# Optimization experiments

Hardware: AMD Instinct MI355X
Metric: run time of the kernel (lower is better)

Reference implementation:

```python
import jax, jax.numpy as jnp
import numpy as np

K = 1024
D = 64
BETA = 0.25


def setup_inputs() -> dict:
    key = jax.random.key(0)
    k1, k2 = jax.random.split(key)
    latents = jax.random.normal(k1, (32, 64, 64, 64), dtype=jnp.float32)  # [B, C=D, H, W]
    # embedding init: uniform(-1/K, 1/K)
    embedding = jax.random.uniform(k2, (K, D), dtype=jnp.float32, minval=-1.0 / K, maxval=1.0 / K)
    return {"latents": latents, "embedding": embedding}


def reference(latents, embedding):
    # [B, D, H, W] -> [B, H, W, D]
    x = jnp.transpose(latents, (0, 2, 3, 1))
    shp = x.shape
    flat = x.reshape(-1, D)  # [N, D]

    dist = (jnp.sum(flat ** 2, axis=1, keepdims=True)
            + jnp.sum(embedding ** 2, axis=1)
            - 2.0 * flat @ embedding.T)  # [N, K]
    inds = jnp.argmin(dist, axis=1)  # [N]

    quantized = embedding[inds].reshape(shp)  # gather == one-hot @ embedding

    commitment_loss = jnp.mean((jax.lax.stop_gradient(quantized) - x) ** 2)
    embedding_loss = jnp.mean((quantized - jax.lax.stop_gradient(x)) ** 2)
    vq_loss = commitment_loss * BETA + embedding_loss

    # straight-through estimator
    quantized = x + jax.lax.stop_gradient(quantized - x)
    out = jnp.transpose(quantized, (0, 3, 1, 2))  # back to [B, D, H, W]
    return out, vq_loss
```

## Files before the change

### kernel.cpp

```cpp
#include <hip/hip_runtime.h>
#include <hip/hip_bf16.h>


#define HW 4096
#define OUTELEMS 8388608

typedef __attribute__((ext_vector_type(8))) short bf16x8;
typedef __attribute__((ext_vector_type(4))) float f32x4;
typedef __attribute__((ext_vector_type(4))) int i32x4;

static __device__ __forceinline__ short f2bf(float f) {
    union { __hip_bfloat16 h; short s; } u;
    u.h = __float2bfloat16(f);
    return u.s;
}
static __device__ __forceinline__ unsigned umin2(unsigned a, unsigned b) {
    return a < b ? a : b;
}


__global__ __launch_bounds__(256) void prep_kernel(const float* __restrict__ emb,
                                                   short* __restrict__ Ebf,
                                                   float* __restrict__ en1,
                                                   float* __restrict__ loss) {
    int code = blockIdx.x * 4 + (threadIdx.x >> 6);
    int d = threadIdx.x & 63;
    float v = emb[code * 64 + d];
    int g = d >> 3, j = d & 7;
    Ebf[code * 64 + ((g + code) & 7) * 8 + j] = f2bf(-2.0f * v);
    float s = v * v;
#pragma unroll
    for (int off = 32; off > 0; off >>= 1) s += __shfl_xor(s, off, 64);
    if (d == 0) en1[code] = 1.0f + s;
    if (blockIdx.x == 0 && threadIdx.x == 0) *loss = 0.0f;
}

__global__ __launch_bounds__(512, 2) void vq_kernel(
        const float* __restrict__ lat, const short* __restrict__ Ebf,
        const float* __restrict__ en1, float* __restrict__ out,
        float* __restrict__ loss) {
    extern __shared__ __align__(16) char sbuf[];
    const int tid  = threadIdx.x;
    const int wave = tid >> 6;
    const int lane = tid & 63;
    const int n    = lane & 15;
    const int quad = lane >> 4;

    const int g0 = blockIdx.x * 512;
    const int b  = g0 >> 12;
    const int mb = g0 & 4095;
    const float* latb = lat + (size_t)b * 262144;

    {
        const f32x4* src = (const f32x4*)Ebf;
        f32x4* dst = (f32x4*)sbuf;
#pragma unroll
        for (int r = 0; r < 16; ++r)
            dst[r * 512 + tid] = src[r * 512 + tid];
        if (tid < 256)
            ((f32x4*)(sbuf + 131072))[tid] = ((const f32x4*)en1)[tid];
    }

    bf16x8 bfr[4][2];
    float xnorm[4];
#pragma unroll
    for (int s = 0; s < 4; ++s) {
        const float* xp = latb + (mb + wave * 64 + s * 16 + n);
        float xs = 0.0f; bf16x8 f0, f1;
#pragma unroll
        for (int j = 0; j < 8; ++j) {
            float x0 = xp[(quad * 8 + j) * HW];
            float x1 = xp[(32 + quad * 8 + j) * HW];
            xs += x0 * x0 + x1 * x1;
            f0[j] = f2bf(x0); f1[j] = f2bf(x1);
        }
        bfr[s][0] = f0; bfr[s][1] = f1; xnorm[s] = xs;
    }
    __syncthreads();

    const int slot0 = ((quad + n) & 7) * 16;
    const int slot1 = ((quad + 4 + n) & 7) * 16;
    const char* arowBase = sbuf + n * 128;
    const f32x4* enl = (const f32x4*)(sbuf + 131072);
    unsigned emin[4] = {0xFFFFFFFFu, 0xFFFFFFFFu, 0xFFFFFFFFu, 0xFFFFFFFFu};

#pragma unroll 2
    for (int ct = 0; ct < 64; ++ct) {
        const char* rb = arowBase + ct * 2048;
        bf16x8 a0 = *(const bf16x8*)(rb + slot0);
        bf16x8 a1 = *(const bf16x8*)(rb + slot1);
        f32x4 en4 = enl[ct * 4 + quad];
        const unsigned cb = ct * 16 + quad * 4;
#pragma unroll
        for (int s = 0; s < 4; ++s) {
            f32x4 acc = __builtin_amdgcn_mfma_f32_16x16x32_bf16(a0, bfr[s][0], en4, 0, 0, 0);
            acc = __builtin_amdgcn_mfma_f32_16x16x32_bf16(a1, bfr[s][1], acc, 0, 0, 0);
            unsigned e0 = (__float_as_uint(acc[0]) & 0xFFFFFC00u) | (cb + 0);
            unsigned e1 = (__float_as_uint(acc[1]) & 0xFFFFFC00u) | (cb + 1);
            unsigned e2 = (__float_as_uint(acc[2]) & 0xFFFFFC00u) | (cb + 2);
            unsigned e3 = (__float_as_uint(acc[3]) & 0xFFFFFC00u) | (cb + 3);
            emin[s] = umin2(emin[s], umin2(umin2(e0, e1), umin2(e2, e3)));
        }
    }

#pragma unroll
    for (int off = 16; off <= 32; off <<= 1) {
#pragma unroll
        for (int s = 0; s < 4; ++s) {
            unsigned eo = (unsigned)__shfl_xor((int)emin[s], off, 64);
            float xo = __shfl_xor(xnorm[s], off, 64);
            emin[s] = eo < emin[s] ? eo : emin[s];
            xnorm[s] += xo;
        }
    }

    int* codes = (int*)(sbuf + 135168);
    if (quad == 0) {
#pragma unroll
        for (int s = 0; s < 4; ++s)
            codes[wave * 64 + s * 16 + n] = (int)(emin[s] & 1023u);
    }

    float contrib = 0.0f;
#pragma unroll
    for (int s = 0; s < 4; ++s)
        contrib += __uint_as_float(emin[s] & 0xFFFFFC00u) - 1.0f + xnorm[s];
#pragma unroll
    for (int off = 32; off > 0; off >>= 1) contrib += __shfl_xor(contrib, off, 64);
    float* wsum = (float*)(sbuf + 137216);
    if (lane == 0) wsum[wave] = contrib;
    __syncthreads();
    if (tid == 0) {
        float t = 0.0f;
#pragma unroll
        for (int w = 0; w < 8; ++w) t += wsum[w];
        atomicAdd(loss, t * (1.25f / (8388608.0f * 4.0f)));
    }

    float* outb = out + (size_t)b * 262144 + mb;
#pragma unroll 2
    for (int i = 0; i < 16; ++i) {
        int id = i * 512 + tid;
        int d  = id >> 7;
        int mq = (id & 127) * 4;
        i32x4 c4 = *(const i32x4*)(codes + mq);
        int g = d >> 3, j2 = (d & 7) * 2;
        unsigned u0 = *(const unsigned short*)(sbuf + c4.x * 128 + ((g + c4.x) & 7) * 16 + j2);
        unsigned u1 = *(const unsigned short*)(sbuf + c4.y * 128 + ((g + c4.y) & 7) * 16 + j2);
        unsigned u2 = *(const unsigned short*)(sbuf + c4.z * 128 + ((g + c4.z) & 7) * 16 + j2);
        unsigned u3 = *(const unsigned short*)(sbuf + c4.w * 128 + ((g + c4.w) & 7) * 16 + j2);
        f32x4 v;
        v[0] = __uint_as_float(u0 << 16) * -0.5f;
        v[1] = __uint_as_float(u1 << 16) * -0.5f;
        v[2] = __uint_as_float(u2 << 16) * -0.5f;
        v[3] = __uint_as_float(u3 << 16) * -0.5f;
        *(f32x4*)(outb + d * HW + mq) = v;
    }
}

extern "C" void kernel_launch(void* const* d_in, const int* in_sizes, int n_in,
                              void* d_out, int out_size, void* d_ws, size_t ws_size,
                              hipStream_t stream) {
    const float* latents   = (const float*)d_in[0];
    const float* embedding = (const float*)d_in[1];
    float* out  = (float*)d_out;
    float* loss = out + OUTELEMS;

    char* ws = (char*)d_ws;
    short* Ebf = (short*)ws;
    float* en1 = (float*)(ws + 131072);

    hipFuncSetAttribute((const void*)vq_kernel,
                        hipFuncAttributeMaxDynamicSharedMemorySize, 137280);

    prep_kernel<<<256, 256, 0, stream>>>(embedding, Ebf, en1, loss);
    vq_kernel<<<256, 512, 137280, stream>>>(latents, Ebf, en1, out, loss);
}
```

Measured before the change: 108.1 us.

## Use 1024-thread blocks with fewer points per wave and paired-row epilogue

Doubles the block to 16 waves, each handling 32 latent points instead of 64, so more waves per CU share the single LDS-resident codebook and can hide latency. The gather/store epilogue now reads two adjacent bf16 codebook values with one 32-bit LDS load and writes two output rows per iteration. The loss atomic is moved after the output stores. In exchange, each A-fragment LDS read is reused across fewer MFMAs, and the tighter launch bounds (1024,4) may cap registers hard enough to cause spills.

```diff
diff --git a/kernel.cpp b/kernel.cpp
--- a/kernel.cpp
+++ b/kernel.cpp
@@ -35,7 +35,7 @@
     if (blockIdx.x == 0 && threadIdx.x == 0) *loss = 0.0f;
 }
 
-__global__ __launch_bounds__(512, 2) void vq_kernel(
+__global__ __launch_bounds__(1024, 4) void vq_kernel(
         const float* __restrict__ lat, const short* __restrict__ Ebf,
         const float* __restrict__ en1, float* __restrict__ out,
         float* __restrict__ loss) {
@@ -55,17 +55,17 @@
         const f32x4* src = (const f32x4*)Ebf;
         f32x4* dst = (f32x4*)sbuf;
 #pragma unroll
-        for (int r = 0; r < 16; ++r)
-            dst[r * 512 + tid] = src[r * 512 + tid];
+        for (int r = 0; r < 8; ++r)
+            dst[r * 1024 + tid] = src[r * 1024 + tid];
         if (tid < 256)
             ((f32x4*)(sbuf + 131072))[tid] = ((const f32x4*)en1)[tid];
     }
 
-    bf16x8 bfr[4][2];
-    float xnorm[4];
+    bf16x8 bfr[2][2];
+    float xnorm[2];
 #pragma unroll
-    for (int s = 0; s < 4; ++s) {
-        const float* xp = latb + (mb + wave * 64 + s * 16 + n);
+    for (int s = 0; s < 2; ++s) {
+        const float* xp = latb + (mb + wave * 32 + s * 16 + n);
         float xs = 0.0f; bf16x8 f0, f1;
 #pragma unroll
         for (int j = 0; j < 8; ++j) {
@@ -82,7 +82,7 @@
     const int slot1 = ((quad + 4 + n) & 7) * 16;
     const char* arowBase = sbuf + n * 128;
     const f32x4* enl = (const f32x4*)(sbuf + 131072);
-    unsigned emin[4] = {0xFFFFFFFFu, 0xFFFFFFFFu, 0xFFFFFFFFu, 0xFFFFFFFFu};
+    unsigned emin[2] = {0xFFFFFFFFu, 0xFFFFFFFFu};
 
 #pragma unroll 2
     for (int ct = 0; ct < 64; ++ct) {
@@ -92,21 +92,21 @@
         f32x4 en4 = enl[ct * 4 + quad];
         const unsigned cb = ct * 16 + quad * 4;
 #pragma unroll
-        for (int s = 0; s < 4; ++s) {
+        for (int s = 0; s < 2; ++s) {
             f32x4 acc = __builtin_amdgcn_mfma_f32_16x16x32_bf16(a0, bfr[s][0], en4, 0, 0, 0);
             acc = __builtin_amdgcn_mfma_f32_16x16x32_bf16(a1, bfr[s][1], acc, 0, 0, 0);
             unsigned e0 = (__float_as_uint(acc[0]) & 0xFFFFFC00u) | (cb + 0);
             unsigned e1 = (__float_as_uint(acc[1]) & 0xFFFFFC00u) | (cb + 1);
             unsigned e2 = (__float_as_uint(acc[2]) & 0xFFFFFC00u) | (cb + 2);
             unsigned e3 = (__float_as_uint(acc[3]) & 0xFFFFFC00u) | (cb + 3);
-            emin[s] = umin2(emin[s], umin2(umin2(e0, e1), umin2(e2, e3)));
+            emin[s] = umin2(umin2(umin2(umin2(e0, e1), e2), e3), emin[s]);
         }
     }
 
 #pragma unroll
     for (int off = 16; off <= 32; off <<= 1) {
 #pragma unroll
-        for (int s = 0; s < 4; ++s) {
+        for (int s = 0; s < 2; ++s) {
             unsigned eo = (unsigned)__shfl_xor((int)emin[s], off, 64);
             float xo = __shfl_xor(xnorm[s], off, 64);
             emin[s] = eo < emin[s] ? eo : emin[s];
@@ -116,45 +116,51 @@
 
     int* codes = (int*)(sbuf + 135168);
     if (quad == 0) {
-#pragma unroll
-        for (int s = 0; s < 4; ++s)
-            codes[wave * 64 + s * 16 + n] = (int)(emin[s] & 1023u);
+        codes[wave * 32 + n]      = (int)(emin[0] & 1023u);
+        codes[wave * 32 + 16 + n] = (int)(emin[1] & 1023u);
     }
 
     float contrib = 0.0f;
 #pragma unroll
-    for (int s = 0; s < 4; ++s)
+    for (int s = 0; s < 2; ++s)
         contrib += __uint_as_float(emin[s] & 0xFFFFFC00u) - 1.0f + xnorm[s];
 #pragma unroll
     for (int off = 32; off > 0; off >>= 1) contrib += __shfl_xor(contrib, off, 64);
     float* wsum = (float*)(sbuf + 137216);
     if (lane == 0) wsum[wave] = contrib;
     __syncthreads();
+
+    float* outb = out + (size_t)b * 262144 + mb;
+#pragma unroll 2
+    for (int i = 0; i < 4; ++i) {
+        int id = i * 1024 + tid;
+        int dp = id >> 7;
+        int d  = dp * 2;
+        int mq = (id & 127) * 4;
+        i32x4 c4 = *(const i32x4*)(codes + mq);
+        int g = d >> 3, j2 = (d & 7) * 2;
+        unsigned u0 = *(const unsigned*)(sbuf + c4.x * 128 + ((g + c4.x) & 7) * 16 + j2);
+        unsigned u1 = *(const unsigned*)(sbuf + c4.y * 128 + ((g + c4.y) & 7) * 16 + j2);
+        unsigned u2 = *(const unsigned*)(sbuf + c4.z * 128 + ((g + c4.z) & 7) * 16 + j2);
+        unsigned u3 = *(const unsigned*)(sbuf + c4.w * 128 + ((g + c4.w) & 7) * 16 + j2);
+        f32x4 vlo, vhi;
+        vlo[0] = __uint_as_float(u0 << 16) * -0.5f;
+        vlo[1] = __uint_as_float(u1 << 16) * -0.5f;
+        vlo[2] = __uint_as_float(u2 << 16) * -0.5f;
+        vlo[3] = __uint_as_float(u3 << 16) * -0.5f;
+        vhi[0] = __uint_as_float(u0 & 0xFFFF0000u) * -0.5f;
+        vhi[1] = __uint_as_float(u1 & 0xFFFF0000u) * -0.5f;
+        vhi[2] = __uint_as_float(u2 & 0xFFFF0000u) * -0.5f;
+        vhi[3] = __uint_as_float(u3 & 0xFFFF0000u) * -0.5f;
+        *(f32x4*)(outb + d * HW + mq)       = vlo;
+        *(f32x4*)(outb + (d + 1) * HW + mq) = vhi;
+    }
+
     if (tid == 0) {
         float t = 0.0f;
 #pragma unroll
-        for (int w = 0; w < 8; ++w) t += wsum[w];
+        for (int w = 0; w < 16; ++w) t += wsum[w];
         atomicAdd(loss, t * (1.25f / (8388608.0f * 4.0f)));
-    }
-
-    float* outb = out + (size_t)b * 262144 + mb;
-#pragma unroll 2
-    for (int i = 0; i < 16; ++i) {
-        int id = i * 512 + tid;
-        int d  = id >> 7;
-        int mq = (id & 127) * 4;
-        i32x4 c4 = *(const i32x4*)(codes + mq);
-        int g = d >> 3, j2 = (d & 7) * 2;
-        unsigned u0 = *(const unsigned short*)(sbuf + c4.x * 128 + ((g + c4.x) & 7) * 16 + j2);
-        unsigned u1 = *(const unsigned short*)(sbuf + c4.y * 128 + ((g + c4.y) & 7) * 16 + j2);
-        unsigned u2 = *(const unsigned short*)(sbuf + c4.z * 128 + ((g + c4.z) & 7) * 16 + j2);
-        unsigned u3 = *(const unsigned short*)(sbuf + c4.w * 128 + ((g + c4.w) & 7) * 16 + j2);
-        f32x4 v;
-        v[0] = __uint_as_float(u0 << 16) * -0.5f;
-        v[1] = __uint_as_float(u1 << 16) * -0.5f;
-        v[2] = __uint_as_float(u2 << 16) * -0.5f;
-        v[3] = __uint_as_float(u3 << 16) * -0.5f;
-        *(f32x4*)(outb + d * HW + mq) = v;
     }
 }
 
@@ -174,5 +180,5 @@
                         hipFuncAttributeMaxDynamicSharedMemorySize, 137280);
 
     prep_kernel<<<256, 256, 0, stream>>>(embedding, Ebf, en1, loss);
-    vq_kernel<<<256, 512, 137280, stream>>>(latents, Ebf, en1, out, loss);
+    vq_kernel<<<256, 1024, 137280, stream>>>(latents, Ebf, en1, out, loss);
 }
```

New measurement: 104.4 us (median of 2 runs). -3.4%, faster.
